# Performance work log

Measured on AMD Instinct MI355X. Metric: run time of the kernel, lower is better.

The kernel has to match this reference:

```python
import math
import jax, jax.numpy as jnp
import numpy as np

B, T, E, H = 8, 2048, 512, 8
NQ_H, NL = 4, 2          # qubits per attention head, circuit layers
NQ_F, FFN = 8, 2048      # FFN qubits, ffn_dim

# ---- batched state-vector quantum simulation -------------------------------
# state shape: [N, 2, 2, ..., 2] (one axis of size 2 per qubit; wire q = axis q+1)

def apply_ry(state, q, theta):
    """RY(theta) on wire q. theta: scalar or [N] (per-batch angle)."""
    th = jnp.asarray(theta) * 0.5
    c, s = jnp.cos(th), jnp.sin(th)
    if th.ndim == 1:
        shp = (-1,) + (1,) * (state.ndim - 2)
        c, s = c.reshape(shp), s.reshape(shp)
    s0 = jax.lax.index_in_dim(state, 0, axis=q + 1, keepdims=False)
    s1 = jax.lax.index_in_dim(state, 1, axis=q + 1, keepdims=False)
    return jnp.stack([c * s0 - s * s1, s * s0 + c * s1], axis=q + 1)

def apply_cnot(state, ctrl, tgt):
    c0 = jax.lax.index_in_dim(state, 0, axis=ctrl + 1, keepdims=True)
    c1 = jax.lax.index_in_dim(state, 1, axis=ctrl + 1, keepdims=True)
    c1 = jnp.flip(c1, axis=tgt + 1)  # X on target when control = 1
    return jnp.concatenate([c0, c1], axis=ctrl + 1)

def run_circuit(x, params):
    """x: [N, n] data angles. params: [L, n] (shared) or [N, L, n] (per-element).
    Circuit: L x (RY(params) layer + CNOT chain + ring CNOT), then RY(x), then <Z_q>.
    Returns [N, n] PauliZ expectations."""
    N, n = x.shape
    L = params.shape[-2]
    state = jnp.zeros((N, 2 ** n), x.dtype).at[:, 0].set(1.0).reshape((N,) + (2,) * n)
    for l in range(L):
        for q in range(n):
            theta = params[:, l, q] if params.ndim == 3 else params[l, q]
            state = apply_ry(state, q, theta)
        for q in range(n - 1):
            state = apply_cnot(state, q, q + 1)
        state = apply_cnot(state, n - 1, 0)
    for q in range(n):
        state = apply_ry(state, q, x[:, q])
    probs = (state ** 2).reshape(N, 2 ** n)
    bits = (jnp.arange(2 ** n)[:, None] >> (n - 1 - jnp.arange(n))) & 1  # wire 0 = MSB
    return probs @ (1 - 2 * bits).astype(x.dtype)  # [N, n]

def layer_norm(x, g, b, eps=1e-5):
    m = x.mean(-1, keepdims=True)
    v = ((x - m) ** 2).mean(-1, keepdims=True)
    return (x - m) / jnp.sqrt(v + eps) * g + b

def setup_inputs() -> dict:
    key = jax.random.key(0)
    ks = jax.random.split(key, 9)
    def lin(k, o, i):
        return jax.random.normal(k, (o, i), jnp.float32) / np.sqrt(i).astype(np.float32)
    return {
        "x": jax.random.normal(ks[0], (B, T, E), jnp.float32),
        "wq": lin(ks[1], E, E), "wk": lin(ks[2], E, E),
        "wv": lin(ks[3], E, E), "wo": lin(ks[4], E, E),
        "head_params": jax.random.normal(ks[5], (H, NL, NQ_H), jnp.float32),
        "ffn_params": jax.random.normal(ks[6], (2, NQ_F), jnp.float32),
        "w1": lin(ks[7], FFN, NQ_F), "w2": lin(ks[8], E, FFN),
        "g1": jnp.ones((E,), jnp.float32), "b1": jnp.zeros((E,), jnp.float32),
        "g2": jnp.ones((E,), jnp.float32), "b2": jnp.zeros((E,), jnp.float32),
    }

def reference(x, wq, wk, wv, wo, head_params, ffn_params, w1, w2, g1, b1, g2, b2):
    Bb, Tt, Ee = x.shape
    hd = Ee // H
    BT = Bb * Tt
    # ---- quantum multi-head attention (dropout = eval/identity) ----
    q = x @ wq.T; k = x @ wk.T; v = x @ wv.T
    scores = jnp.einsum('bte,bse->bts', q, k) / math.sqrt(Ee)  # NOTE: scale by sqrt(E)
    attn = jax.nn.softmax(scores, axis=-1)
    out = jnp.einsum('bts,bse->bte', attn, v)                  # [B,T,E]
    oh = out.reshape(Bb, Tt, H, hd)
    # fold heads into the batch dim; per-head params broadcast per element
    xh = oh[..., :NQ_H].transpose(2, 0, 1, 3).reshape(H * BT, NQ_H)
    ph = jnp.broadcast_to(head_params[:, None], (H, BT, NL, NQ_H)).reshape(H * BT, NL, NQ_H)
    qout = run_circuit(xh, ph)                                  # [H*BT, NQ_H]
    qout = jnp.pad(qout, ((0, 0), (0, hd - NQ_H)))              # zero-pad to head_dim
    qout = qout.reshape(H, Bb, Tt, hd).transpose(1, 2, 0, 3).reshape(Bb, Tt, Ee)
    attn_out = qout @ wo.T
    x1 = layer_norm(x + attn_out, g1, b1)
    # ---- quantum FFN (only ffn_params[0] used, as in source) ----
    xf = x1.reshape(BT, Ee)[:, :NQ_F]
    f = run_circuit(xf, ffn_params[:1]).reshape(Bb, Tt, NQ_F)
    f = jax.nn.relu(f @ w1.T) @ w2.T
    return layer_norm(x1 + f, g2, b2)
```

## Files before the change

kernel.cpp:

```cpp
#include <hip/hip_runtime.h>
#include <hip/hip_bf16.h>
#include <math.h>


#define B_   8
#define T_   2048
#define E_   512

typedef __attribute__((ext_vector_type(8))) short bf16x8;
typedef __attribute__((ext_vector_type(4))) short bf16x4;
typedef __attribute__((ext_vector_type(4))) float f32x4;

#define GLL16(g, l) __builtin_amdgcn_global_load_lds((const __attribute__((address_space(1))) void*)(g), (__attribute__((address_space(3))) void*)(l), 16, 0, 0)

__device__ inline unsigned short f2bf(float f){
  union { float f; unsigned u; } v; v.f = f;
  unsigned r = v.u + 0x7fff + ((v.u >> 16) & 1);
  return (unsigned short)(r >> 16);
}

__global__ __launch_bounds__(256) void k0_setup(const float* __restrict__ hp,
                         const float* __restrict__ fp,
                         const float* __restrict__ wo, float* __restrict__ cAB,
                         unsigned short* __restrict__ wo32b) {
  int t = threadIdx.x, bi = blockIdx.x;
  if (bi > 0) {
    int gid = (bi-1)*256 + t;
    int e = gid >> 3, c4 = gid & 7;
    float4 v = *(const float4*)(wo + (size_t)e*512 + c4*64);
    unsigned short h[4] = { f2bf(v.x), f2bf(v.y), f2bf(v.z), f2bf(v.w) };
    *(unsigned long long*)(wo32b + (size_t)e*32 + c4*4) = *(unsigned long long*)h;
    return;
  }
  __shared__ float fst[256], tmp[256], ra[256], rb[256];
  fst[t] = (t == 0) ? 1.f : 0.f;
  __syncthreads();
  #pragma unroll
  for (int q = 0; q < 8; ++q) {
    int str = 1 << (7-q);
    float th = 0.5f * fp[q];
    float c = cosf(th), s = sinf(th);
    float self = fst[t], part = fst[t ^ str];
    float nv = (t & str) ? (c*self + s*part) : (c*self - s*part);
    __syncthreads();
    tmp[t] = nv;
    __syncthreads();
    fst[t] = tmp[t];
    __syncthreads();
  }
  #pragma unroll
  for (int g = 0; g < 8; ++g) {
    int ctrl = (g < 7) ? g : 7, tgt = (g < 7) ? g+1 : 0;
    int cs = 1 << (7-ctrl), tsr = 1 << (7-tgt);
    float nv = fst[(t & cs) ? (t ^ tsr) : t];
    __syncthreads();
    fst[t] = nv;
    __syncthreads();
  }
  #pragma unroll
  for (int q = 0; q < 8; ++q) {
    int str = 1 << (7-q);
    float a = fst[t]*fst[t] * ((t & str) ? -1.f : 1.f);
    float b = fst[t]*fst[t ^ str];
    ra[t] = a; rb[t] = b;
    __syncthreads();
    for (int off = 128; off > 0; off >>= 1){
      if (t < off){ ra[t] += ra[t+off]; rb[t] += rb[t+off]; }
      __syncthreads();
    }
    if (t == 0){ cAB[64+q] = ra[0]; cAB[72+q] = rb[0]; }
    __syncthreads();
  }
  if (t < 8) {
    float st[16];
    #pragma unroll
    for (int i=0;i<16;i++) st[i]=0.f;
    st[0]=1.f;
    for (int l=0;l<2;l++){
      for (int q=0;q<4;q++){
        float th = 0.5f*hp[t*8 + l*4 + q];
        float c = cosf(th), s = sinf(th);
        int str = 1<<(3-q);
        for (int i=0;i<16;i++) if (!(i & str)) {
          float s0=st[i], s1=st[i|str];
          st[i]     = c*s0 - s*s1;
          st[i|str] = s*s0 + c*s1;
        }
      }
      for (int q=0;q<4;q++){
        int ctrl = (q<3)? q : 3, tgt = (q<3)? q+1 : 0;
        int cs = 1<<(3-ctrl), tsr = 1<<(3-tgt);
        for (int i=0;i<16;i++) if ((i&cs) && !(i&tsr)) {
          float tt = st[i]; st[i]=st[i|tsr]; st[i|tsr]=tt;
        }
      }
    }
    for (int q=0;q<4;q++){
      int str = 1<<(3-q);
      float A=0.f, Bv=0.f;
      for (int i=0;i<16;i++){
        A  += st[i]*st[i] * ((i&str)? -1.f : 1.f);
        Bv += st[i]*st[i^str];
      }
      cAB[t*4+q]    = A;
      cAB[32+t*4+q] = Bv;
    }
  }
}

__global__ __launch_bounds__(256) void kc_cast(const float* __restrict__ x,
                     const float* __restrict__ wq, const float* __restrict__ wk,
                     const float* __restrict__ w2, const float* __restrict__ wv,
                     unsigned short* __restrict__ xb, unsigned short* __restrict__ wqkb,
                     unsigned short* __restrict__ w2b, unsigned short* __restrict__ wv32b){
  int bi = blockIdx.x;
  if (bi < 4096) {
    int i = bi*256 + threadIdx.x;
    const float4* p = (const float4*)x + (size_t)i*2;
    float4 a = p[0], b = p[1];
    union { unsigned short h[8]; uint4 u; } o;
    o.h[0]=f2bf(a.x); o.h[1]=f2bf(a.y); o.h[2]=f2bf(a.z); o.h[3]=f2bf(a.w);
    o.h[4]=f2bf(b.x); o.h[5]=f2bf(b.y); o.h[6]=f2bf(b.z); o.h[7]=f2bf(b.w);
    ((uint4*)xb)[i] = o.u;
    return;
  }
  int i = (bi-4096)*256 + threadIdx.x;
  const float* src; unsigned short* dst; float s = 1.f;
  if (i < 65536){
    int row = i >> 6, c8 = (i & 63)*8;
    if (row < 512){ src = wq + (size_t)row*512 + c8; s = 0.044194173824159216f; }
    else          { src = wk + (size_t)(row-512)*512 + c8; }
    dst = wqkb + (size_t)row*512 + c8;
  } else if (i < 196608){
    int j = i - 65536;
    src = w2 + (size_t)j*8; dst = w2b + (size_t)j*8;
  } else {
    int j = i - 196608;
    int r = j >> 6, c8 = (j & 63)*8;
    src = wv + (size_t)((r>>2)*64 + (r&3))*512 + c8;
    dst = wv32b + (size_t)r*512 + c8;
  }
  float4 a = *(const float4*)src, b = *(const float4*)(src+4);
  union { unsigned short h[8]; uint4 u; } o;
  o.h[0]=f2bf(a.x*s); o.h[1]=f2bf(a.y*s); o.h[2]=f2bf(a.z*s); o.h[3]=f2bf(a.w*s);
  o.h[4]=f2bf(b.x*s); o.h[5]=f2bf(b.y*s); o.h[6]=f2bf(b.z*s); o.h[7]=f2bf(b.w*s);
  *(uint4*)dst = o.u;
}

template<int K, int LDC, bool OUTBF, int GX, int GM>
__global__ __launch_bounds__(256,2) void gemm_bt(
    const unsigned short* __restrict__ A, const unsigned short* __restrict__ Bw,
    void* __restrict__ C, int m_base){
  __shared__ __align__(16) char sm[16384];
  char* As = sm; char* Bs = sm + 8192;
  int t = threadIdx.x, w = t>>6, l = t&63;
  int lr = l&15, quad = l>>4;
  int lin = blockIdx.x;
  int n0 = ((lin >> 3) % GX) * 128;
  int m0 = ((lin & 7) * (GM/8) + lin / (8*GX)) * 128;
  int wr = (w>>1)*64, wc = (w&1)*64;
  f32x4 acc[4][4] = {};
  for (int k0 = 0; k0 < K; k0 += 32){
    __syncthreads();
    #pragma unroll
    for (int c = 0; c < 2; ++c){
      int ch = c*256 + t, row = ch>>2, sw = ch&3, lc = sw ^ ((row>>1)&3);
      GLL16(A  + (size_t)(m0+row)*K + k0 + lc*8, As + c*4096 + w*1024);
      GLL16(Bw + (size_t)(n0+row)*K + k0 + lc*8, Bs + c*4096 + w*1024);
    }
    __syncthreads();
    bf16x8 af[4], bg[4];
    #pragma unroll
    for (int i=0;i<4;++i){
      int ra = wr + i*16 + lr;
      af[i] = *(const bf16x8*)(As + ra*64 + (quad ^ ((ra>>1)&3))*16);
      int rb = wc + i*16 + lr;
      bg[i] = *(const bf16x8*)(Bs + rb*64 + (quad ^ ((rb>>1)&3))*16);
    }
    #pragma unroll
    for (int i=0;i<4;++i)
      #pragma unroll
      for (int j=0;j<4;++j)
        acc[i][j] = __builtin_amdgcn_mfma_f32_16x16x32_bf16(af[i], bg[j], acc[i][j], 0,0,0);
  }
  #pragma unroll
  for (int i=0;i<4;++i)
    #pragma unroll
    for (int j=0;j<4;++j)
      #pragma unroll
      for (int r=0;r<4;++r){
        size_t row = (size_t)(m_base + m0 + wr + i*16 + quad*4 + r);
        int col = n0 + wc + j*16 + lr;
        if constexpr (OUTBF) ((unsigned short*)C)[row*LDC + col] = f2bf(acc[i][j][r]);
        else                 ((float*)C)[row*LDC + col] = acc[i][j][r];
      }
}

__global__ __launch_bounds__(256) void k1_v32m(const unsigned short* __restrict__ xb,
    const unsigned short* __restrict__ wv32b, unsigned short* __restrict__ v32t){
  __shared__ __align__(16) char sm1[98304];
  char* Xs = sm1; char* Ws = sm1 + 65536;
  int t = threadIdx.x, w = t>>6, l = t&63, lr = l&15, quad = l>>4;
  int m0 = blockIdx.x * 64;
  #pragma unroll
  for (int i=0;i<16;++i){
    int p = i*256 + t, ks = p>>8, c2 = p&255, row = c2>>2, swp = c2&3;
    int lc = swp ^ ((row>>1)&3);
    GLL16(xb + (size_t)(m0+row)*512 + ks*32 + lc*8, Xs + (p>>6)*1024);
  }
  #pragma unroll
  for (int i=0;i<8;++i){
    int p = i*256 + t, ks = p>>7, c2 = p&127, row = c2>>2, swp = c2&3;
    int lc = swp ^ ((row>>1)&3);
    GLL16(wv32b + (size_t)row*512 + ks*32 + lc*8, Ws + (p>>6)*1024);
  }
  __syncthreads();
  f32x4 acc[2] = {};
  #pragma unroll
  for (int ks=0; ks<16; ++ks){
    int xrow = w*16 + lr;
    bf16x8 bq = *(const bf16x8*)(Xs + ks*4096 + xrow*64 + (quad ^ ((xrow>>1)&3))*16);
    #pragma unroll
    for (int ni=0; ni<2; ++ni){
      int wrow = ni*16 + lr;
      bf16x8 af = *(const bf16x8*)(Ws + ks*2048 + wrow*64 + (quad ^ ((wrow>>1)&3))*16);
      acc[ni] = __builtin_amdgcn_mfma_f32_16x16x32_bf16(af, bq, acc[ni], 0,0,0);
    }
  }
  int bb = m0 >> 11, sbase = (m0 & 2047) + w*16 + lr;
  #pragma unroll
  for (int ni=0; ni<2; ++ni)
    #pragma unroll
    for (int r=0; r<4; ++r){
      int c = ni*16 + quad*4 + r;
      v32t[((size_t)(bb*32 + c))*2048 + sbase] = f2bf(acc[ni][r]);
    }
}

__global__ __launch_bounds__(256,2) void k2_attn(
    const unsigned short* __restrict__ qkb, const unsigned short* __restrict__ v32t,
    float* __restrict__ Opart, float* __restrict__ mlb){
  __shared__ __align__(16) char sm[77824];
  char* Qc  = sm;
  char* Ks  = sm + 16384;
  char* Vts = sm + 49152;
  float* OtL = (float*)sm;
  float* mL  = (float*)(sm + 73728);
  float* lL  = (float*)(sm + 75776);

  int t = threadIdx.x, w = t>>6, l = t&63;
  int lr = l & 15, quad = l >> 4;
  int lin = blockIdx.x;
  int b = lin & 7;
  int m0 = ((lin >> 3) & 15) * 128;
  int half = lin >> 7;
  size_t bT = (size_t)b*2048;
  const char* qbase = (const char*)qkb + (bT + m0)*2048;
  const char* vbase = (const char*)v32t + (size_t)b*32*4096;

  f32x4 Ot[2][8] = {};
  float mold[8], lsum[8];
  #pragma unroll
  for (int qj=0;qj<8;++qj){ mold[qj] = -1e30f; lsum[qj] = 0.f; }

  for (int st = 0; st < 2; ++st){
    int s0 = (half*2 + st)*256;
    const char* kbase = (const char*)qkb + (bT + s0)*2048 + 1024;
    __syncthreads();
    {
      int j = t>>3, seg = t&7;
      const uint4* vs = (const uint4*)(vbase + (size_t)j*4096 + (s0 + seg*32)*2);
      uint4* vd = (uint4*)(Vts + j*528 + seg*64);
      vd[0]=vs[0]; vd[1]=vs[1]; vd[2]=vs[2]; vd[3]=vs[3];
    }
    f32x4 acc[4][8] = {};
    for (int ec = 0; ec < 8; ++ec){
      __syncthreads();
      #pragma unroll
      for (int u = 0; u < 4; ++u){
        int kk = u>>1, c = u&1;
        int ch = c*256 + t, row = ch>>2, sw = ch&3, lc = sw ^ ((row>>1)&3);
        GLL16(qbase + (size_t)row*2048 + ec*128 + kk*64 + lc*16,
              Qc + kk*8192 + c*4096 + w*1024);
      }
      #pragma unroll
      for (int rd = 0; rd < 4; ++rd){
        int ch = rd*256 + t, row = ch>>2, sw = ch&3, lc = sw ^ ((row>>1)&3);
        GLL16(kbase + (size_t)row*2048 + ec*128 +      lc*16, Ks +         rd*4096 + w*1024);
        GLL16(kbase + (size_t)row*2048 + ec*128 + 64 + lc*16, Ks + 16384 + rd*4096 + w*1024);
      }
      __syncthreads();
      #pragma unroll
      for (int kk = 0; kk < 2; ++kk){
        bf16x8 af[4];
        #pragma unroll
        for (int si = 0; si < 4; ++si){
          int row = w*64 + si*16 + lr;
          af[si] = *(const bf16x8*)(Ks + kk*16384 + row*64 + (quad ^ ((row>>1)&3))*16);
        }
        #pragma unroll
        for (int qh = 0; qh < 2; ++qh){
          bf16x8 bq[4];
          #pragma unroll
          for (int jj = 0; jj < 4; ++jj){
            int row = (qh*4+jj)*16 + lr;
            bq[jj] = *(const bf16x8*)(Qc + kk*8192 + row*64 + (quad ^ ((row>>1)&3))*16);
          }
          __builtin_amdgcn_s_setprio(1);
          #pragma unroll
          for (int si = 0; si < 4; ++si)
            #pragma unroll
            for (int jj = 0; jj < 4; ++jj)
              acc[si][qh*4+jj] = __builtin_amdgcn_mfma_f32_16x16x32_bf16(af[si], bq[jj], acc[si][qh*4+jj], 0,0,0);
          __builtin_amdgcn_s_setprio(0);
        }
      }
    }
    bf16x4 aV[2][4];
    #pragma unroll
    for (int vt=0; vt<2; ++vt)
      #pragma unroll
      for (int si=0; si<4; ++si)
        aV[vt][si] = *(const bf16x4*)(Vts + (vt*16+lr)*528 + (w*64 + si*16 + quad*4)*2);
    #pragma unroll
    for (int qj=0; qj<8; ++qj){
      float mt = -1e30f;
      #pragma unroll
      for (int si=0; si<4; ++si)
        #pragma unroll
        for (int r=0;r<4;++r) mt = fmaxf(mt, acc[si][qj][r]);
      mt = fmaxf(mt, __shfl_xor(mt, 16));
      mt = fmaxf(mt, __shfl_xor(mt, 32));
      float mn = fmaxf(mold[qj], mt);
      float al = __expf(mold[qj] - mn);
      mold[qj] = mn;
      float rs = 0.f;
      #pragma unroll
      for (int si=0; si<4; ++si)
        #pragma unroll
        for (int r=0;r<4;++r){
          float p = __expf(acc[si][qj][r] - mn);
          acc[si][qj][r] = p; rs += p;
        }
      rs += __shfl_xor(rs, 16); rs += __shfl_xor(rs, 32);
      lsum[qj] = lsum[qj]*al + rs;
      Ot[0][qj] *= al; Ot[1][qj] *= al;
      #pragma unroll
      for (int si=0; si<4; ++si){
        bf16x4 pb;
        pb[0]=(short)f2bf(acc[si][qj][0]); pb[1]=(short)f2bf(acc[si][qj][1]);
        pb[2]=(short)f2bf(acc[si][qj][2]); pb[3]=(short)f2bf(acc[si][qj][3]);
        Ot[0][qj] = __builtin_amdgcn_mfma_f32_16x16x16bf16_1k(aV[0][si], pb, Ot[0][qj], 0,0,0);
        Ot[1][qj] = __builtin_amdgcn_mfma_f32_16x16x16bf16_1k(aV[1][si], pb, Ot[1][qj], 0,0,0);
      }
    }
  }
  __syncthreads();
  #pragma unroll
  for (int qj=0; qj<8; ++qj){
    if (quad == 0){ mL[w*128 + qj*16 + lr] = mold[qj]; lL[w*128 + qj*16 + lr] = lsum[qj]; }
    *(f32x4*)(OtL + (size_t)(w*128 + qj*16 + lr)*36 + quad*4)      = Ot[0][qj];
    *(f32x4*)(OtL + (size_t)(w*128 + qj*16 + lr)*36 + 16 + quad*4) = Ot[1][qj];
  }
  __syncthreads();
  #pragma unroll
  for (int u=0; u<2; ++u){
    int qr = u*64 + (t>>2), vg = (t&3)*8;
    float M = -1e30f;
    #pragma unroll
    for (int w4=0; w4<4; ++w4) M = fmaxf(M, mL[w4*128+qr]);
    float L = 0.f; float o[8] = {};
    #pragma unroll
    for (int w4=0; w4<4; ++w4){
      float a = __expf(mL[w4*128+qr] - M);
      L += a * lL[w4*128+qr];
      const float* Op = OtL + (size_t)(w4*128+qr)*36 + vg;
      #pragma unroll
      for (int j=0;j<8;++j) o[j] += a*Op[j];
    }
    size_t tok = bT + m0 + qr;
    float* od = Opart + ((size_t)half*16384 + tok)*32 + vg;
    *(float4*)od     = make_float4(o[0],o[1],o[2],o[3]);
    *(float4*)(od+4) = make_float4(o[4],o[5],o[6],o[7]);
    if ((t&3) == 0){
      mlb[((size_t)half*16384 + tok)*2]     = M;
      mlb[((size_t)half*16384 + tok)*2 + 1] = L;
    }
  }
}

__global__ __launch_bounds__(256) void k2_merge(const float* __restrict__ Opart,
    const float* __restrict__ mlb, const float* __restrict__ cAB,
    unsigned short* __restrict__ q32b){
  int g = blockIdx.x*256 + threadIdx.x;
  int tok = g >> 2, vg = (g & 3) * 8;
  float m[4], lv[4];
  #pragma unroll
  for (int h=0;h<4;++h){
    m[h]  = mlb[((size_t)h*16384 + tok)*2];
    lv[h] = mlb[((size_t)h*16384 + tok)*2 + 1];
  }
  float M = fmaxf(fmaxf(m[0],m[1]), fmaxf(m[2],m[3]));
  float a[4], L = 0.f;
  #pragma unroll
  for (int h=0;h<4;++h){ a[h] = __expf(m[h]-M); L += a[h]*lv[h]; }
  float inv = 1.f / L;
  float o[8] = {};
  #pragma unroll
  for (int h=0;h<4;++h){
    const float* O = Opart + ((size_t)h*16384 + tok)*32 + vg;
    #pragma unroll
    for (int j=0;j<8;++j) o[j] += a[h]*O[j];
  }
  union { unsigned short h[8]; uint4 u; } res;
  #pragma unroll
  for (int j=0;j<8;++j){
    float ov = o[j] * inv;
    int cc = vg + j;
    res.h[j] = f2bf(cosf(ov)*cAB[cc] - sinf(ov)*cAB[32+cc]);
  }
  *(uint4*)(q32b + (size_t)tok*32 + vg) = res.u;
}

__global__ __launch_bounds__(256) void k3_proj_ln(const float* __restrict__ x,
    const unsigned short* __restrict__ q32b, const unsigned short* __restrict__ wo32b,
    const float* __restrict__ g1, const float* __restrict__ b1,
    const float* __restrict__ cAB, float* __restrict__ x1, float* __restrict__ fbuf) {
  __shared__ __align__(16) char sm3[36224];
  char* Ws = sm3;
  char* Qs = sm3 + 32768;
  float* red1 = (float*)(sm3 + 34816);
  float* red2 = (float*)(sm3 + 35328);
  float* mm   = (float*)(sm3 + 35840);
  float* rr   = (float*)(sm3 + 35968);
  int t = threadIdx.x, w = t>>6, l = t&63, lr = l&15, quad = l>>4;
  int tok0 = blockIdx.x * 32;
  #pragma unroll
  for (int i=0;i<8;++i){
    int g = t + i*256, row = g>>2, ch = g&3;
    uint4 v = ((const uint4*)wo32b)[g];
    *(uint4*)(Ws + row*64 + (ch ^ ((row>>1)&3))*16) = v;
  }
  if (t < 128){
    int row = t>>2, ch = t&3;
    uint4 v = ((const uint4*)(q32b + (size_t)tok0*32))[t];
    *(uint4*)(Qs + row*64 + (ch ^ ((row>>1)&3))*16) = v;
  }
  __syncthreads();
  bf16x8 af[2], bf[8];
  #pragma unroll
  for (int i=0;i<2;++i){
    int m = i*16 + lr;
    af[i] = *(const bf16x8*)(Qs + m*64 + (quad ^ ((m>>1)&3))*16);
  }
  #pragma unroll
  for (int j=0;j<8;++j){
    int n = w*128 + j*16 + lr;
    bf[j] = *(const bf16x8*)(Ws + n*64 + (quad ^ ((n>>1)&3))*16);
  }
  f32x4 acc[2][8];
  #pragma unroll
  for (int i=0;i<2;++i)
    #pragma unroll
    for (int j=0;j<8;++j){
      f32x4 z = {0.f,0.f,0.f,0.f};
      acc[i][j] = __builtin_amdgcn_mfma_f32_16x16x32_bf16(af[i], bf[j], z, 0,0,0);
    }
  float s1[2][4] = {}, s2[2][4] = {};
  #pragma unroll
  for (int i=0;i<2;++i)
    #pragma unroll
    for (int r=0;r<4;++r){
      int m = i*16 + quad*4 + r;
      const float* xrow = x + (size_t)(tok0+m)*512 + w*128 + lr;
      #pragma unroll
      for (int j=0;j<8;++j){
        float v = acc[i][j][r] + xrow[j*16];
        acc[i][j][r] = v;
        s1[i][r] += v; s2[i][r] += v*v;
      }
    }
  #pragma unroll
  for (int off=1; off<16; off<<=1){
    #pragma unroll
    for (int i=0;i<2;++i)
      #pragma unroll
      for (int r=0;r<4;++r){
        s1[i][r] += __shfl_xor(s1[i][r], off);
        s2[i][r] += __shfl_xor(s2[i][r], off);
      }
  }
  if (lr == 0){
    #pragma unroll
    for (int i=0;i<2;++i)
      #pragma unroll
      for (int r=0;r<4;++r){
        int m = i*16 + quad*4 + r;
        red1[w*32 + m] = s1[i][r];
        red2[w*32 + m] = s2[i][r];
      }
  }
  __syncthreads();
  if (t < 32){
    float a = red1[t] + red1[32+t] + red1[64+t] + red1[96+t];
    float bb = red2[t] + red2[32+t] + red2[64+t] + red2[96+t];
    float mean = a * (1.f/512.f);
    float var  = bb * (1.f/512.f) - mean*mean;
    mm[t] = mean; rr[t] = rsqrtf(var + 1e-5f);
  }
  __syncthreads();
  float g1v[8], b1v[8];
  #pragma unroll
  for (int j=0;j<8;++j){
    int n = w*128 + j*16 + lr;
    g1v[j] = g1[n]; b1v[j] = b1[n];
  }
  #pragma unroll
  for (int i=0;i<2;++i)
    #pragma unroll
    for (int r=0;r<4;++r){
      int m = i*16 + quad*4 + r;
      float mean = mm[m], rstd = rr[m];
      float* orow = x1 + (size_t)(tok0+m)*512 + w*128 + lr;
      #pragma unroll
      for (int j=0;j<8;++j){
        float nv = (acc[i][j][r]-mean)*rstd*g1v[j] + b1v[j];
        orow[j*16] = nv;
        if (w == 0 && j == 0 && lr < 8)
          fbuf[(size_t)(tok0+m)*8 + lr] = cosf(nv)*cAB[64+lr] - sinf(nv)*cAB[72+lr];
      }
    }
}

__global__ __launch_bounds__(256) void k4a4(const float* __restrict__ fbuf,
    const float* __restrict__ w1, unsigned short* __restrict__ Hb, int row0){
  __shared__ float w1s[16384];
  int t = threadIdx.x;
  #pragma unroll
  for (int i=0;i<16;++i){
    int p = i*256 + t;
    *(float4*)(w1s + (size_t)p*4) = *(const float4*)(w1 + (size_t)p*4);
  }
  __syncthreads();
  float wv[8][8];
  #pragma unroll
  for (int i=0;i<16;++i){
    float4 v = *(const float4*)(w1s + t*64 + i*4);
    wv[i>>1][(i&1)*4+0]=v.x; wv[i>>1][(i&1)*4+1]=v.y;
    wv[i>>1][(i&1)*4+2]=v.z; wv[i>>1][(i&1)*4+3]=v.w;
  }
  int tokL = blockIdx.x * 32;
  #pragma unroll 2
  for (int u=0;u<32;++u){
    const float4* fp4 = (const float4*)(fbuf + (size_t)(row0 + tokL + u)*8);
    float4 fa = fp4[0], fb = fp4[1];
    union { unsigned short h[8]; uint4 q; } o;
    #pragma unroll
    for (int j=0;j<8;++j){
      float s = fa.x*wv[j][0] + fa.y*wv[j][1] + fa.z*wv[j][2] + fa.w*wv[j][3]
              + fb.x*wv[j][4] + fb.y*wv[j][5] + fb.z*wv[j][6] + fb.w*wv[j][7];
      o.h[j] = f2bf(fmaxf(s, 0.f));
    }
    *(uint4*)(Hb + (size_t)(tokL + u)*2048 + t*8) = o.q;
  }
}

__global__ __launch_bounds__(256) void k5_ln2(const float* __restrict__ x1,
    const float* __restrict__ g2, const float* __restrict__ b2,
    float* __restrict__ out) {
  int tok = blockIdx.x, t = threadIdx.x;
  __shared__ float rs1[4], rs2[4], mv[2];
  float vals[2], ssum=0.f, ssq=0.f;
  #pragma unroll
  for (int u=0;u<2;u++){
    int e = t + u*256;
    float s = x1[(size_t)tok*512 + e] + out[(size_t)tok*512 + e];
    vals[u]=s; ssum+=s; ssq+=s*s;
  }
  #pragma unroll
  for (int off=32; off>0; off>>=1){ ssum += __shfl_down(ssum,off); ssq += __shfl_down(ssq,off); }
  int wid = t >> 6;
  if ((t & 63) == 0){ rs1[wid]=ssum; rs2[wid]=ssq; }
  __syncthreads();
  if (t == 0){
    float a = rs1[0]+rs1[1]+rs1[2]+rs1[3];
    float b = rs2[0]+rs2[1]+rs2[2]+rs2[3];
    float mean = a * (1.f/512.f);
    float var  = b * (1.f/512.f) - mean*mean;
    mv[0]=mean; mv[1]=rsqrtf(var + 1e-5f);
  }
  __syncthreads();
  float mean=mv[0], rstd=mv[1];
  #pragma unroll
  for (int u=0;u<2;u++){
    int e = t + u*256;
    out[(size_t)tok*512 + e] = (vals[u]-mean)*rstd*g2[e] + b2[e];
  }
}

extern "C" void kernel_launch(void* const* d_in, const int* in_sizes, int n_in,
                              void* d_out, int out_size, void* d_ws, size_t ws_size,
                              hipStream_t stream) {
  const float* x  = (const float*)d_in[0];
  const float* wq = (const float*)d_in[1];
  const float* wk = (const float*)d_in[2];
  const float* wv = (const float*)d_in[3];
  const float* wo = (const float*)d_in[4];
  const float* hp = (const float*)d_in[5];
  const float* fp = (const float*)d_in[6];
  const float* w1 = (const float*)d_in[7];
  const float* w2 = (const float*)d_in[8];
  const float* g1 = (const float*)d_in[9];
  const float* b1 = (const float*)d_in[10];
  const float* g2 = (const float*)d_in[11];
  const float* b2 = (const float*)d_in[12];
  float* out = (float*)d_out;
  float* ws  = (float*)d_ws;

  unsigned short* qkb  = (unsigned short*)(ws);
  float*          x1   = ws + 8388608;
  unsigned short* xb   = (unsigned short*)(ws + 16777216);
  unsigned short* wqkb = (unsigned short*)(ws + 20971520);
  unsigned short* w2b  = (unsigned short*)(ws + 21233664);
  unsigned short* v32t = (unsigned short*)(ws + 21757952);
  unsigned short* q32b = (unsigned short*)(ws + 22020096);
  float*          fbuf = ws + 22544384;
  unsigned short* wo32b= (unsigned short*)(ws + 22675456);
  float*          cAB  = ws + 22691840;
  float*          mlb  = ws + 22691968;
  unsigned short* wv32b= (unsigned short*)(ws + 23806080);
  float*          Opart= ws + 16777216;
  unsigned short* Hb   = (unsigned short*)(ws);

  k0_setup<<<17, 256, 0, stream>>>(hp, fp, wo, cAB, wo32b);
  kc_cast<<<4872, 256, 0, stream>>>(x, wq, wk, w2, wv, xb, wqkb, w2b, wv32b);
  gemm_bt<512,1024,true,8,128><<<1024, 256, 0, stream>>>(xb, wqkb, qkb, 0);
  k1_v32m<<<256, 256, 0, stream>>>(xb, wv32b, v32t);
  k2_attn<<<512, 256, 0, stream>>>(qkb, v32t, Opart, mlb);
  k2_merge<<<256, 256, 0, stream>>>(Opart, mlb, cAB, q32b);
  k3_proj_ln<<<512, 256, 0, stream>>>(x, q32b, wo32b, g1, b1, cAB, x1, fbuf);
  k4a4<<<256, 256, 0, stream>>>(fbuf, w1, Hb, 0);
  gemm_bt<2048,512,false,4,64><<<256, 256, 0, stream>>>(Hb, w2b, out, 0);
  k4a4<<<256, 256, 0, stream>>>(fbuf, w1, Hb, 8192);
  gemm_bt<2048,512,false,4,64><<<256, 256, 0, stream>>>(Hb, w2b, out, 8192);
  k5_ln2<<<16384, 256, 0, stream>>>(x1, g2, b2, out);
}
```

Baseline: 378.3 us.

## Double-buffer QK tile loads in attention and fuse split merge into projection

```diff
diff --git a/kernel.cpp b/kernel.cpp
--- a/kernel.cpp
+++ b/kernel.cpp
@@ -273,48 +273,57 @@
       uint4* vd = (uint4*)(Vts + j*528 + seg*64);
       vd[0]=vs[0]; vd[1]=vs[1]; vd[2]=vs[2]; vd[3]=vs[3];
     }
-    f32x4 acc[4][8] = {};
-    for (int ec = 0; ec < 8; ++ec){
-      __syncthreads();
-      #pragma unroll
-      for (int u = 0; u < 4; ++u){
-        int kk = u>>1, c = u&1;
+    {
+      #pragma unroll
+      for (int c = 0; c < 2; ++c){
         int ch = c*256 + t, row = ch>>2, sw = ch&3, lc = sw ^ ((row>>1)&3);
-        GLL16(qbase + (size_t)row*2048 + ec*128 + kk*64 + lc*16,
-              Qc + kk*8192 + c*4096 + w*1024);
+        GLL16(qbase + (size_t)row*2048 + lc*16, Qc + c*4096 + w*1024);
       }
       #pragma unroll
       for (int rd = 0; rd < 4; ++rd){
         int ch = rd*256 + t, row = ch>>2, sw = ch&3, lc = sw ^ ((row>>1)&3);
-        GLL16(kbase + (size_t)row*2048 + ec*128 +      lc*16, Ks +         rd*4096 + w*1024);
-        GLL16(kbase + (size_t)row*2048 + ec*128 + 64 + lc*16, Ks + 16384 + rd*4096 + w*1024);
-      }
-      __syncthreads();
-      #pragma unroll
-      for (int kk = 0; kk < 2; ++kk){
-        bf16x8 af[4];
+        GLL16(kbase + (size_t)row*2048 + lc*16, Ks + rd*4096 + w*1024);
+      }
+    }
+    f32x4 acc[4][8] = {};
+    __syncthreads();
+    for (int ec = 0; ec < 16; ++ec){
+      int cur = ec&1, nxt = cur^1;
+      if (ec < 15){
         #pragma unroll
-        for (int si = 0; si < 4; ++si){
-          int row = w*64 + si*16 + lr;
-          af[si] = *(const bf16x8*)(Ks + kk*16384 + row*64 + (quad ^ ((row>>1)&3))*16);
+        for (int c = 0; c < 2; ++c){
+          int ch = c*256 + t, row = ch>>2, sw = ch&3, lc = sw ^ ((row>>1)&3);
+          GLL16(qbase + (size_t)row*2048 + (ec+1)*64 + lc*16, Qc + nxt*8192 + c*4096 + w*1024);
         }
         #pragma unroll
-        for (int qh = 0; qh < 2; ++qh){
-          bf16x8 bq[4];
+        for (int rd = 0; rd < 4; ++rd){
+          int ch = rd*256 + t, row = ch>>2, sw = ch&3, lc = sw ^ ((row>>1)&3);
+          GLL16(kbase + (size_t)row*2048 + (ec+1)*64 + lc*16, Ks + nxt*16384 + rd*4096 + w*1024);
+        }
+      }
+      bf16x8 af[4];
+      #pragma unroll
+      for (int si = 0; si < 4; ++si){
+        int row = w*64 + si*16 + lr;
+        af[si] = *(const bf16x8*)(Ks + cur*16384 + row*64 + (quad ^ ((row>>1)&3))*16);
+      }
+      #pragma unroll
+      for (int qh = 0; qh < 2; ++qh){
+        bf16x8 bq[4];
+        #pragma unroll
+        for (int jj = 0; jj < 4; ++jj){
+          int row = (qh*4+jj)*16 + lr;
+          bq[jj] = *(const bf16x8*)(Qc + cur*8192 + row*64 + (quad ^ ((row>>1)&3))*16);
+        }
+        __builtin_amdgcn_s_setprio(1);
+        #pragma unroll
+        for (int si = 0; si < 4; ++si)
           #pragma unroll
-          for (int jj = 0; jj < 4; ++jj){
-            int row = (qh*4+jj)*16 + lr;
-            bq[jj] = *(const bf16x8*)(Qc + kk*8192 + row*64 + (quad ^ ((row>>1)&3))*16);
-          }
-          __builtin_amdgcn_s_setprio(1);
-          #pragma unroll
-          for (int si = 0; si < 4; ++si)
-            #pragma unroll
-            for (int jj = 0; jj < 4; ++jj)
-              acc[si][qh*4+jj] = __builtin_amdgcn_mfma_f32_16x16x32_bf16(af[si], bq[jj], acc[si][qh*4+jj], 0,0,0);
-          __builtin_amdgcn_s_setprio(0);
-        }
-      }
+          for (int jj = 0; jj < 4; ++jj)
+            acc[si][qh*4+jj] = __builtin_amdgcn_mfma_f32_16x16x32_bf16(af[si], bq[jj], acc[si][qh*4+jj], 0,0,0);
+        __builtin_amdgcn_s_setprio(0);
+      }
+      __syncthreads();
     }
     bf16x4 aV[2][4];
     #pragma unroll
@@ -389,41 +398,9 @@
   }
 }
 
-__global__ __launch_bounds__(256) void k2_merge(const float* __restrict__ Opart,
-    const float* __restrict__ mlb, const float* __restrict__ cAB,
-    unsigned short* __restrict__ q32b){
-  int g = blockIdx.x*256 + threadIdx.x;
-  int tok = g >> 2, vg = (g & 3) * 8;
-  float m[4], lv[4];
-  #pragma unroll
-  for (int h=0;h<4;++h){
-    m[h]  = mlb[((size_t)h*16384 + tok)*2];
-    lv[h] = mlb[((size_t)h*16384 + tok)*2 + 1];
-  }
-  float M = fmaxf(fmaxf(m[0],m[1]), fmaxf(m[2],m[3]));
-  float a[4], L = 0.f;
-  #pragma unroll
-  for (int h=0;h<4;++h){ a[h] = __expf(m[h]-M); L += a[h]*lv[h]; }
-  float inv = 1.f / L;
-  float o[8] = {};
-  #pragma unroll
-  for (int h=0;h<4;++h){
-    const float* O = Opart + ((size_t)h*16384 + tok)*32 + vg;
-    #pragma unroll
-    for (int j=0;j<8;++j) o[j] += a[h]*O[j];
-  }
-  union { unsigned short h[8]; uint4 u; } res;
-  #pragma unroll
-  for (int j=0;j<8;++j){
-    float ov = o[j] * inv;
-    int cc = vg + j;
-    res.h[j] = f2bf(cosf(ov)*cAB[cc] - sinf(ov)*cAB[32+cc]);
-  }
-  *(uint4*)(q32b + (size_t)tok*32 + vg) = res.u;
-}
-
 __global__ __launch_bounds__(256) void k3_proj_ln(const float* __restrict__ x,
-    const unsigned short* __restrict__ q32b, const unsigned short* __restrict__ wo32b,
+    const float* __restrict__ Opart, const float* __restrict__ mlb,
+    const unsigned short* __restrict__ wo32b,
     const float* __restrict__ g1, const float* __restrict__ b1,
     const float* __restrict__ cAB, float* __restrict__ x1, float* __restrict__ fbuf) {
   __shared__ __align__(16) char sm3[36224];
@@ -441,10 +418,34 @@
     uint4 v = ((const uint4*)wo32b)[g];
     *(uint4*)(Ws + row*64 + (ch ^ ((row>>1)&3))*16) = v;
   }
-  if (t < 128){
-    int row = t>>2, ch = t&3;
-    uint4 v = ((const uint4*)(q32b + (size_t)tok0*32))[t];
-    *(uint4*)(Qs + row*64 + (ch ^ ((row>>1)&3))*16) = v;
+  {
+    int tokL = t>>3, cg = t&7;
+    size_t gt = (size_t)tok0 + tokL;
+    float m[4], lv[4];
+    #pragma unroll
+    for (int h=0;h<4;++h){
+      m[h]  = mlb[((size_t)h*16384 + gt)*2];
+      lv[h] = mlb[((size_t)h*16384 + gt)*2 + 1];
+    }
+    float M = fmaxf(fmaxf(m[0],m[1]), fmaxf(m[2],m[3]));
+    float a[4], L = 0.f;
+    #pragma unroll
+    for (int h=0;h<4;++h){ a[h] = __expf(m[h]-M); L += a[h]*lv[h]; }
+    float inv = 1.f / L;
+    float o[4] = {};
+    #pragma unroll
+    for (int h=0;h<4;++h){
+      float4 v = *(const float4*)(Opart + ((size_t)h*16384 + gt)*32 + cg*4);
+      o[0] += a[h]*v.x; o[1] += a[h]*v.y; o[2] += a[h]*v.z; o[3] += a[h]*v.w;
+    }
+    bf16x4 qv;
+    #pragma unroll
+    for (int j=0;j<4;++j){
+      float ov = o[j] * inv;
+      int cc = cg*4 + j;
+      qv[j] = (short)f2bf(cosf(ov)*cAB[cc] - sinf(ov)*cAB[32+cc]);
+    }
+    *(bf16x4*)(Qs + tokL*64 + (((cg>>1) ^ ((tokL>>1)&3))<<4) + ((cg&1)<<3)) = qv;
   }
   __syncthreads();
   bf16x8 af[2], bf[8];
@@ -623,7 +624,6 @@
   unsigned short* wqkb = (unsigned short*)(ws + 20971520);
   unsigned short* w2b  = (unsigned short*)(ws + 21233664);
   unsigned short* v32t = (unsigned short*)(ws + 21757952);
-  unsigned short* q32b = (unsigned short*)(ws + 22020096);
   float*          fbuf = ws + 22544384;
   unsigned short* wo32b= (unsigned short*)(ws + 22675456);
   float*          cAB  = ws + 22691840;
@@ -637,8 +637,7 @@
   gemm_bt<512,1024,true,8,128><<<1024, 256, 0, stream>>>(xb, wqkb, qkb, 0);
   k1_v32m<<<256, 256, 0, stream>>>(xb, wv32b, v32t);
   k2_attn<<<512, 256, 0, stream>>>(qkb, v32t, Opart, mlb);
-  k2_merge<<<256, 256, 0, stream>>>(Opart, mlb, cAB, q32b);
-  k3_proj_ln<<<512, 256, 0, stream>>>(x, q32b, wo32b, g1, b1, cAB, x1, fbuf);
+  k3_proj_ln<<<512, 256, 0, stream>>>(x, Opart, mlb, wo32b, g1, b1, cAB, x1, fbuf);
   k4a4<<<256, 256, 0, stream>>>(fbuf, w1, Hb, 0);
   gemm_bt<2048,512,false,4,64><<<256, 256, 0, stream>>>(Hb, w2b, out, 0);
   k4a4<<<256, 256, 0, stream>>>(fbuf, w1, Hb, 8192);
```

After: 392.2 us. 3.7% more time.
